# Kernel optimization log

Measured on AMD Instinct MI355X. Metric: run time of the kernel, lower is better.

## Reference

```python
import jax, jax.numpy as jnp
import numpy as np

N = 16384
N_IN = 64
N_H = 64
DIMS = [N_IN, N_H + 200, N_H + 100, N_H]  # 64 -> 264 -> 164 -> 64 (args.l == 2 path)


def setup_inputs() -> dict:
    key = jax.random.key(0)
    ks = jax.random.split(key, 16)
    inp = {
        "seq1": jax.random.normal(ks[0], (1, N, N_IN), dtype=jnp.float32),
        "seq2": jax.random.normal(ks[1], (1, N, N_IN), dtype=jnp.float32),
        # dense adjacency, scaled ~1/n like a row-normalized GCN adjacency
        "adj": jax.random.uniform(ks[2], (1, N, N), dtype=jnp.float32) / N,
        "samp_bias1": jnp.zeros((1, N), dtype=jnp.float32),
        "samp_bias2": jnp.zeros((1, N), dtype=jnp.float32),
    }
    # GCN layer params: Linear(in, out, bias=False) weight + per-layer bias
    for i in range(3):
        din, dout = DIMS[i], DIMS[i + 1]
        inp[f"w{i+1}"] = jax.random.normal(ks[3 + 2 * i], (din, dout), dtype=jnp.float32) * (1.0 / np.sqrt(din))
        inp[f"b{i+1}"] = jnp.zeros((dout,), dtype=jnp.float32)
    # Discriminator bilinear f_k = nn.Bilinear(n_h, n_h, 1): weight [n_h, n_h], bias scalar
    inp["wd"] = jax.random.normal(ks[10], (N_H, N_H), dtype=jnp.float32) * (1.0 / np.sqrt(N_H))
    inp["bd"] = jnp.zeros((), dtype=jnp.float32)
    return inp


def _encoder(seq, adj, ws, bs):
    h = seq  # [1, n, d]
    for w, b in zip(ws, bs):
        # GCN layer: act(adj @ (X W) + b)
        h = jax.nn.relu(jnp.einsum('bnm,bmd->bnd', adj, jnp.einsum('bnk,kd->bnd', h, w)) + b)
    return h


def reference(seq1, seq2, adj, samp_bias1, samp_bias2, w1, b1, w2, b2, w3, b3, wd, bd):
    ws, bs = (w1, w2, w3), (b1, b2, b3)
    h_1 = _encoder(seq1, adj, ws, bs)                 # [1, n, n_h]
    c = jax.nn.sigmoid(jnp.mean(h_1, axis=1))         # AvgReadout + sigmoid -> [1, n_h]
    h_2 = _encoder(seq2, adj, ws, bs)                 # [1, n, n_h]
    # Bilinear discriminator: sc[b, i] = h[b, i, :] @ Wd @ c[b, :] + bd (+ samp_bias)
    cw = jnp.einsum('bd,ed->be', c, wd)               # Wd acts on (h, c) pair -> [1, n_h]
    sc_1 = jnp.einsum('bnd,bd->bn', h_1, cw) + bd + samp_bias1
    sc_2 = jnp.einsum('bnd,bd->bn', h_2, cw) + bd + samp_bias2
    return jnp.concatenate([sc_1, sc_2], axis=1)      # [1, 2n]
```

## Files before the change

### kernel.cpp

```cpp
#include <hip/hip_runtime.h>
#include <hip/hip_bf16.h>

#define NN 16384

using f32x4  = __attribute__((ext_vector_type(4))) float;
using bf16x8 = __attribute__((ext_vector_type(8))) __bf16;
using u16x8  = __attribute__((ext_vector_type(8))) unsigned short;

__device__ __forceinline__ void gload_lds16(const void* g, void* l) {
  __builtin_amdgcn_global_load_lds(
      (const __attribute__((address_space(1))) unsigned*)g,
      (__attribute__((address_space(3))) unsigned*)l, 16, 0, 0);
}

__device__ __forceinline__ unsigned short bf16r(float x) {
  return __builtin_bit_cast(unsigned short, (__bf16)x);
}

__global__ void zero_cs(float* __restrict__ csS) {
  if (threadIdx.x < 128) csS[threadIdx.x] = 0.f;
}

__global__ void seqsum(const float* __restrict__ seq1, const float* __restrict__ seq2,
                       float* __restrict__ csS) {
  const int e = blockIdx.x >> 4, chunk = blockIdx.x & 15;
  const float* seq = e ? seq2 : seq1;
  const int g = threadIdx.x >> 4;
  const int q = threadIdx.x & 15;
  f32x4 acc = {};
  for (int i = 0; i < 64; ++i) {
    int r = chunk * 1024 + i * 16 + g;
    acc += *(const f32x4*)(seq + (long)r * 64 + q * 4);
  }
  __shared__ f32x4 red[256];
  red[threadIdx.x] = acc;
  __syncthreads();
  if (threadIdx.x < 64) {
    int d = threadIdx.x;
    float s = 0.f;
    #pragma unroll
    for (int g2 = 0; g2 < 16; ++g2) {
      f32x4 v = red[g2 * 16 + (d >> 2)];
      s += v[d & 3];
    }
    atomicAdd(&csS[e * 64 + d], s);
  }
}

__global__ void prep_seq(const float* __restrict__ seq1, const float* __restrict__ seq2,
                         unsigned short* __restrict__ Shi) {
  const int tid = threadIdx.x;
  const int r0  = blockIdx.x * 64;
  const float* seq = blockIdx.y ? seq2 : seq1;
  __shared__ float t[64][65];
  #pragma unroll
  for (int i = 0; i < 16; ++i) {
    int row = i * 4 + (tid >> 6);
    t[row][tid & 63] = seq[(long)(r0 + row) * 64 + (tid & 63)];
  }
  __syncthreads();
  #pragma unroll
  for (int i = 0; i < 16; ++i) {
    int col = i * 4 + (tid >> 6);
    int rr  = tid & 63;
    Shi[(long)(blockIdx.y * 64 + col) * NN + r0 + rr] = bf16r(t[rr][col]);
  }
}

__launch_bounds__(256, 3)
__global__ void gemm1(const float* __restrict__ A,
                      const unsigned short* __restrict__ Xg,
                      const float* __restrict__ cs,
                      float* __restrict__ P,
                      unsigned short* __restrict__ Vg) {
  __shared__ unsigned short As[128 * 64];
  __shared__ unsigned short Xs[2][128 * 64];
  const int tid  = threadIdx.x;
  const int lane = tid & 63;
  const int wave = tid >> 6;
  const int wr = wave & 1;
  const int wc = wave >> 1;

  int bid = blockIdx.x;
  int lin = (bid & 7) * ((int)gridDim.x >> 3) + (bid >> 3);
  const int bx = lin & 127;
  const int bz = lin >> 7;
  const int rtile = bx * 128;
  const int kbase = bz * 4096;

  const int arow0  = wave * 32 + (lane >> 3);
  const int ac     = lane & 7;
  const int awslot = ac ^ (lane >> 3);
  const float* aptr = A + (long)(rtile + arow0) * NN + kbase + ac * 8;
  unsigned short* vptr = Vg + (long)(rtile + arow0) * NN + kbase + ac * 8;

  const int cx = (lane & 7) ^ (lane >> 3);
  const unsigned short* xptr = Xg + (long)arow0 * NN + kbase + cx * 8;

  f32x4 acc[4][4] = {};
  f32x4 areg[4][2];

  #pragma unroll
  for (int t = 0; t < 4; ++t) {
    const float* ap = aptr + (long)t * 8 * NN;
    areg[t][0] = *(const f32x4*)ap;
    areg[t][1] = *(const f32x4*)(ap + 4);
    gload_lds16(xptr + (long)t * 8 * NN, &Xs[0][(wave * 4 + t) * 512]);
  }
  aptr += 64; xptr += 64;
  __syncthreads();

  int cur = 0;
  const int nsteps = 4096 / 64;
  for (int ks = 0; ks < nsteps; ++ks) {
    u16x8 wv[4];
    #pragma unroll
    for (int t = 0; t < 4; ++t) {
      #pragma unroll
      for (int i = 0; i < 8; ++i) {
        float a = (i < 4) ? areg[t][0][i] : areg[t][1][i - 4];
        wv[t][i] = bf16r(fmaf(a, 16384.f, -0.5f));
      }
      *(u16x8*)(vptr + (long)t * 8 * NN) = wv[t];
    }
    vptr += 64;
    __syncthreads();
    #pragma unroll
    for (int t = 0; t < 4; ++t)
      *(u16x8*)&As[(arow0 + t * 8) * 64 + awslot * 8] = wv[t];
    if (ks + 1 < nsteps) {
      #pragma unroll
      for (int t = 0; t < 4; ++t) {
        gload_lds16(xptr + (long)t * 8 * NN, &Xs[cur ^ 1][(wave * 4 + t) * 512]);
        const float* ap = aptr + (long)t * 8 * NN;
        areg[t][0] = *(const f32x4*)ap;
        areg[t][1] = *(const f32x4*)(ap + 4);
      }
      aptr += 64; xptr += 64;
    }
    __syncthreads();
    #pragma unroll
    for (int mk = 0; mk < 2; ++mk) {
      bf16x8 af[4];
      #pragma unroll
      for (int ni = 0; ni < 4; ++ni) {
        int ar = wr * 64 + ni * 16 + (lane & 15);
        int slot = (mk * 4 + (lane >> 4)) ^ (ar & 7);
        af[ni] = *(const bf16x8*)&As[ar * 64 + slot * 8];
      }
      #pragma unroll
      for (int mi = 0; mi < 4; ++mi) {
        int xr = wc * 64 + mi * 16 + (lane & 15);
        int slot = (mk * 4 + (lane >> 4)) ^ (xr & 7);
        bf16x8 xf = *(const bf16x8*)&Xs[cur][xr * 64 + slot * 8];
        #pragma unroll
        for (int ni = 0; ni < 4; ++ni)
          acc[mi][ni] = __builtin_amdgcn_mfma_f32_16x16x32_bf16(xf, af[ni], acc[mi][ni], 0, 0, 0);
      }
    }
    cur ^= 1;
  }

  const float scl = 1.f / 16384.f;
  float* out = P + (long)bz * 128 * NN;
  #pragma unroll
  for (int mi = 0; mi < 4; ++mi) {
    int xc = wc * 64 + mi * 16 + ((lane >> 4) << 2);
    float dc[4];
    #pragma unroll
    for (int j = 0; j < 4; ++j) dc[j] = (bz == 0) ? 0.5f * cs[xc + j] : 0.f;
    #pragma unroll
    for (int ni = 0; ni < 4; ++ni) {
      int ar = rtile + wr * 64 + ni * 16 + (lane & 15);
      #pragma unroll
      for (int j = 0; j < 4; ++j)
        out[(long)(xc + j) * NN + ar] = (acc[mi][ni][j] + dc[j]) * scl;
    }
  }
}

__launch_bounds__(256, 3)
__global__ void gemm23(const unsigned short* __restrict__ Va,
                       const unsigned short* __restrict__ Xg,
                       const float* __restrict__ cs,
                       float* __restrict__ P, int ccols, int klen, int nY) {
  __shared__ unsigned short As[128 * 64];
  __shared__ unsigned short Xs[2][128 * 64];
  const int tid  = threadIdx.x;
  const int lane = tid & 63;
  const int wave = tid >> 6;
  const int wr = wave & 1;
  const int wc = wave >> 1;

  int bid = blockIdx.x;
  int lin = (bid & 7) * ((int)gridDim.x >> 3) + (bid >> 3);
  const int by = lin % nY;
  const int bx = (lin / nY) & 127;
  const int bz = lin / (nY * 128);
  const int rtile = bx * 128;
  const int ctile = by * 128;
  const int kbase = bz * klen;

  const int arow0  = wave * 32 + (lane >> 3);
  const int ac     = lane & 7;
  const int awslot = ac ^ (lane >> 3);
  const unsigned short* aptr = Va + (long)(rtile + arow0) * NN + kbase + ac * 8;

  const int cx = (lane & 7) ^ (lane >> 3);
  const unsigned short* xptr = Xg + (long)(ctile + arow0) * NN + kbase + cx * 8;

  f32x4 acc[4][4] = {};
  u16x8 av[4];

  #pragma unroll
  for (int t = 0; t < 4; ++t) {
    av[t] = *(const u16x8*)(aptr + (long)t * 8 * NN);
    gload_lds16(xptr + (long)t * 8 * NN, &Xs[0][(wave * 4 + t) * 512]);
  }
  aptr += 64; xptr += 64;
  __syncthreads();

  int cur = 0;
  const int nsteps = klen / 64;
  for (int ks = 0; ks < nsteps; ++ks) {
    __syncthreads();
    #pragma unroll
    for (int t = 0; t < 4; ++t)
      *(u16x8*)&As[(arow0 + t * 8) * 64 + awslot * 8] = av[t];
    if (ks + 1 < nsteps) {
      #pragma unroll
      for (int t = 0; t < 4; ++t) {
        gload_lds16(xptr + (long)t * 8 * NN, &Xs[cur ^ 1][(wave * 4 + t) * 512]);
        av[t] = *(const u16x8*)(aptr + (long)t * 8 * NN);
      }
      aptr += 64; xptr += 64;
    }
    __syncthreads();
    #pragma unroll
    for (int mk = 0; mk < 2; ++mk) {
      bf16x8 af[4];
      #pragma unroll
      for (int ni = 0; ni < 4; ++ni) {
        int ar = wr * 64 + ni * 16 + (lane & 15);
        int slot = (mk * 4 + (lane >> 4)) ^ (ar & 7);
        af[ni] = *(const bf16x8*)&As[ar * 64 + slot * 8];
      }
      #pragma unroll
      for (int mi = 0; mi < 4; ++mi) {
        int xr = wc * 64 + mi * 16 + (lane & 15);
        int slot = (mk * 4 + (lane >> 4)) ^ (xr & 7);
        bf16x8 xf = *(const bf16x8*)&Xs[cur][xr * 64 + slot * 8];
        #pragma unroll
        for (int ni = 0; ni < 4; ++ni)
          acc[mi][ni] = __builtin_amdgcn_mfma_f32_16x16x32_bf16(xf, af[ni], acc[mi][ni], 0, 0, 0);
      }
    }
    cur ^= 1;
  }

  const float scl = 1.f / 16384.f;
  float* out = P + (long)bz * ccols * NN;
  #pragma unroll
  for (int mi = 0; mi < 4; ++mi) {
    int xc = ctile + wc * 64 + mi * 16 + ((lane >> 4) << 2);
    float dc[4];
    #pragma unroll
    for (int j = 0; j < 4; ++j) dc[j] = (bz == 0) ? 0.5f * cs[xc + j] : 0.f;
    #pragma unroll
    for (int ni = 0; ni < 4; ++ni) {
      int ar = rtile + wr * 64 + ni * 16 + (lane & 15);
      #pragma unroll
      for (int j = 0; j < 4; ++j)
        out[(long)(xc + j) * NN + ar] = (acc[mi][ni][j] + dc[j]) * scl;
    }
  }
}

__global__ void post1a(const float* __restrict__ P, const float* __restrict__ w1,
                       const float* __restrict__ b1, float* __restrict__ H1T) {
  const int r = blockIdx.x * 256 + threadIdx.x;
  const int e = blockIdx.y;
  for (int c = blockIdx.z * 2; c < blockIdx.z * 2 + 2; ++c) {
    const int j0 = c * 66;
    float acc[66];
    #pragma unroll
    for (int jj = 0; jj < 66; ++jj) acc[jj] = b1[j0 + jj];
    for (int k = 0; k < 64; ++k) {
      float tv = 0.f;
      #pragma unroll
      for (int z = 0; z < 4; ++z)
        tv += P[(long)(z * 128 + e * 64 + k) * NN + r];
      #pragma unroll
      for (int jj = 0; jj < 66; ++jj)
        acc[jj] = fmaf(tv, w1[k * 264 + j0 + jj], acc[jj]);
    }
    #pragma unroll
    for (int jj = 0; jj < 66; ++jj)
      H1T[(long)(e * 264 + j0 + jj) * NN + r] = fmaxf(acc[jj], 0.f);
  }
}

__global__ void post1b(const float* __restrict__ H1T, const float* __restrict__ w2,
                       unsigned short* __restrict__ G) {
  const int r  = blockIdx.x * 256 + threadIdx.x;
  const int e  = blockIdx.y;
  const int q0 = blockIdx.z * 41;
  float acc[41] = {};
  for (int j = 0; j < 264; ++j) {
    float h = H1T[(long)(e * 264 + j) * NN + r];
    #pragma unroll
    for (int qq = 0; qq < 41; ++qq)
      acc[qq] = fmaf(h, w2[j * 164 + q0 + qq], acc[qq]);
  }
  #pragma unroll
  for (int qq = 0; qq < 41; ++qq)
    G[(long)(e * 192 + q0 + qq) * NN + r] = bf16r(acc[qq]);
  if (blockIdx.z == 3) {
    for (int q = 164; q < 192; ++q)
      G[(long)(e * 192 + q) * NN + r] = 0;
  }
}

__global__ void colsum_bf16(const unsigned short* __restrict__ X, float* __restrict__ cs) {
  const int c = blockIdx.x;
  const unsigned short* row = X + (long)c * NN;
  float s = 0.f;
  for (int i = threadIdx.x; i < NN; i += 256)
    s += __uint_as_float((unsigned)row[i] << 16);
  __shared__ float red[256];
  red[threadIdx.x] = s;
  __syncthreads();
  for (int off = 128; off > 0; off >>= 1) {
    if (threadIdx.x < off) red[threadIdx.x] += red[threadIdx.x + off];
    __syncthreads();
  }
  if (threadIdx.x == 0) cs[c] = red[0];
}

__global__ void post2(const float* __restrict__ P, const float* __restrict__ w3,
                      const float* __restrict__ b2, unsigned short* __restrict__ F) {
  const int r  = blockIdx.x * 256 + threadIdx.x;
  const int e  = blockIdx.y;
  const int q0 = blockIdx.z * 32;
  float f[32] = {};
  for (int j = 0; j < 164; ++j) {
    float h = P[(long)(e * 192 + j) * NN + r] + P[(long)(384 + e * 192 + j) * NN + r] + b2[j];
    h = fmaxf(h, 0.f);
    #pragma unroll
    for (int q = 0; q < 32; ++q) f[q] = fmaf(h, w3[j * 64 + q0 + q], f[q]);
  }
  #pragma unroll
  for (int q = 0; q < 32; ++q)
    F[(long)(e * 64 + q0 + q) * NN + r] = bf16r(f[q]);
}

__global__ void post3(const float* __restrict__ P, const float* __restrict__ b3,
                      float* __restrict__ H3T) {
  const int r = blockIdx.x * 256 + threadIdx.x;
  const int e = blockIdx.y;
  #pragma unroll
  for (int q = 0; q < 64; ++q) {
    float v = b3[q];
    #pragma unroll
    for (int z = 0; z < 4; ++z)
      v += P[(long)(z * 128 + e * 64 + q) * NN + r];
    H3T[(long)(e * 64 + q) * NN + r] = fmaxf(v, 0.f);
  }
}

__global__ void colsum(const float* __restrict__ H3T, float* __restrict__ sums) {
  const int c = blockIdx.x;
  const float* row = H3T + (long)c * NN;
  float s = 0.f;
  for (int i = threadIdx.x; i < NN; i += 256) s += row[i];
  __shared__ float red[256];
  red[threadIdx.x] = s;
  __syncthreads();
  for (int off = 128; off > 0; off >>= 1) {
    if (threadIdx.x < off) red[threadIdx.x] += red[threadIdx.x + off];
    __syncthreads();
  }
  if (threadIdx.x == 0) sums[c] = red[0];
}

__global__ void make_cw(const float* __restrict__ sums, const float* __restrict__ wd,
                        float* __restrict__ cw) {
  __shared__ float cv[64];
  const int t = threadIdx.x;
  cv[t] = 1.f / (1.f + expf(-sums[t] / 16384.f));
  __syncthreads();
  float a = 0.f;
  for (int d = 0; d < 64; ++d) a += cv[d] * wd[t * 64 + d];
  cw[t] = a;
}

__global__ void score(const float* __restrict__ H3T, const float* __restrict__ cw,
                      const float* __restrict__ bdp, const float* __restrict__ sb1,
                      const float* __restrict__ sb2, float* __restrict__ out) {
  const int idx = blockIdx.x * 256 + threadIdx.x;
  const int e = idx >> 14, r = idx & (NN - 1);
  float acc = bdp[0] + (e ? sb2[r] : sb1[r]);
  const float* base = H3T + (long)e * 64 * NN + r;
  #pragma unroll
  for (int j = 0; j < 64; ++j) acc = fmaf(base[(long)j * NN], cw[j], acc);
  out[idx] = acc;
}

extern "C" void kernel_launch(void* const* d_in, const int* in_sizes, int n_in,
                              void* d_out, int out_size, void* d_ws, size_t ws_size,
                              hipStream_t stream) {
  const float* seq1 = (const float*)d_in[0];
  const float* seq2 = (const float*)d_in[1];
  const float* adj  = (const float*)d_in[2];
  const float* sb1  = (const float*)d_in[3];
  const float* sb2  = (const float*)d_in[4];
  const float* w1   = (const float*)d_in[5];
  const float* b1   = (const float*)d_in[6];
  const float* w2   = (const float*)d_in[7];
  const float* b2   = (const float*)d_in[8];
  const float* w3   = (const float*)d_in[9];
  const float* b3   = (const float*)d_in[10];
  const float* wd   = (const float*)d_in[11];
  const float* bd   = (const float*)d_in[12];
  float* out = (float*)d_out;

  char* ws = (char*)d_ws;
  unsigned short* Vg  = (unsigned short*)(ws + 0);
  unsigned short* Shi = (unsigned short*)(ws + 536870912);
  float*          Pp  = (float*)(ws + 541065216);
  unsigned short* G   = (unsigned short*)(ws + 591396864);
  float*          H1T = (float*)(ws + 603979776);
  unsigned short* F   = (unsigned short*)(ws + 638582784);
  float*          H3T = (float*)(ws + 642777088);
  float*          csS = (float*)(ws + 651165696);
  float*          csG = (float*)(ws + 651166208);
  float*          csF = (float*)(ws + 651167744);
  float*          sums= (float*)(ws + 651168256);
  float*          cw  = (float*)(ws + 651168512);

  zero_cs    <<<1, 128, 0, stream>>>(csS);
  seqsum     <<<32, 256, 0, stream>>>(seq1, seq2, csS);
  prep_seq   <<<dim3(256, 2), 256, 0, stream>>>(seq1, seq2, Shi);
  gemm1      <<<512, 256, 0, stream>>>(adj, Shi, csS, Pp, Vg);
  post1a     <<<dim3(64, 2, 2), 256, 0, stream>>>(Pp, w1, b1, H1T);
  post1b     <<<dim3(64, 2, 4), 256, 0, stream>>>(H1T, w2, G);
  colsum_bf16<<<384, 256, 0, stream>>>(G, csG);
  gemm23     <<<768, 256, 0, stream>>>(Vg, G, csG, Pp, 384, 8192, 3);
  post2      <<<dim3(64, 2, 2), 256, 0, stream>>>(Pp, w3, b2, F);
  colsum_bf16<<<128, 256, 0, stream>>>(F, csF);
  gemm23     <<<512, 256, 0, stream>>>(Vg, F, csF, Pp, 128, 4096, 1);
  post3      <<<dim3(64, 2), 256, 0, stream>>>(Pp, b3, H3T);
  colsum     <<<64, 256, 0, stream>>>(H3T, sums);
  make_cw    <<<1, 64, 0, stream>>>(sums, wd, cw);
  score      <<<128, 256, 0, stream>>>(H3T, cw, bd, sb1, sb2, out);
}
```

Baseline: 1.116 ms.

## Store centered adjacency copy as FP8 and H1T as bf16

gemm1 now writes the re-used, centered and scaled adjacency copy in an 8-bit float format (custom encoder, larger pre-scale) instead of bf16. This halves the dominant HBM traffic when gemm23 re-reads it twice. gemm23 decodes it back to bf16 in registers with packed convert instructions and rescales the result. post1a is restructured to compute the P reduction once per thread and emit bf16 H1T, which shrinks post1b's reads. Precision loss from fp8 storage of the adjacency risks accuracy, and the extra decode work adds ALU cost in the GEMM loop.

```diff
diff --git a/kernel.cpp b/kernel.cpp
--- a/kernel.cpp
+++ b/kernel.cpp
@@ -4,6 +4,7 @@
 #define NN 16384
 
 using f32x4  = __attribute__((ext_vector_type(4))) float;
+using f32x2  = __attribute__((ext_vector_type(2))) float;
 using bf16x8 = __attribute__((ext_vector_type(8))) __bf16;
 using u16x8  = __attribute__((ext_vector_type(8))) unsigned short;
 
@@ -15,6 +16,35 @@
 
 __device__ __forceinline__ unsigned short bf16r(float x) {
   return __builtin_bit_cast(unsigned short, (__bf16)x);
+}
+
+__device__ __forceinline__ unsigned fp8_enc(float f) {
+  unsigned u    = __float_as_uint(f);
+  unsigned sign = (u >> 24) & 0x80u;
+  unsigned mag  = u & 0x7FFFFFFFu;
+  unsigned e32  = mag >> 23;
+  unsigned keep = (mag >> 20) & 7u;
+  unsigned rest = mag & 0xFFFFFu;
+  unsigned r    = ((e32 - 120u) << 3) | keep;
+  r += (rest > 0x80000u) || ((rest == 0x80000u) && (keep & 1u));
+  if (e32 < 121u) r = 0u;
+  return sign | r;
+}
+
+__device__ __forceinline__ u16x8 fp8x8_to_bf16x8(uint2 r) {
+  f32x2 p0, p1, p2, p3;
+  unsigned hx = r.x >> 16, hy = r.y >> 16;
+  asm("v_cvt_pk_f32_fp8 %0, %1" : "=v"(p0) : "v"(r.x));
+  asm("v_cvt_pk_f32_fp8 %0, %1" : "=v"(p1) : "v"(hx));
+  asm("v_cvt_pk_f32_fp8 %0, %1" : "=v"(p2) : "v"(r.y));
+  asm("v_cvt_pk_f32_fp8 %0, %1" : "=v"(p3) : "v"(hy));
+  unsigned q0, q1, q2, q3;
+  asm("v_cvt_pk_bf16_f32 %0, %1, %2" : "=v"(q0) : "v"(p0.x), "v"(p0.y));
+  asm("v_cvt_pk_bf16_f32 %0, %1, %2" : "=v"(q1) : "v"(p1.x), "v"(p1.y));
+  asm("v_cvt_pk_bf16_f32 %0, %1, %2" : "=v"(q2) : "v"(p2.x), "v"(p2.y));
+  asm("v_cvt_pk_bf16_f32 %0, %1, %2" : "=v"(q3) : "v"(p3.x), "v"(p3.y));
+  uint4 qq = {q0, q1, q2, q3};
+  return __builtin_bit_cast(u16x8, qq);
 }
 
 __global__ void zero_cs(float* __restrict__ csS) {
@@ -72,7 +102,7 @@
                       const unsigned short* __restrict__ Xg,
                       const float* __restrict__ cs,
                       float* __restrict__ P,
-                      unsigned short* __restrict__ Vg) {
+                      unsigned char* __restrict__ Vg) {
   __shared__ unsigned short As[128 * 64];
   __shared__ unsigned short Xs[2][128 * 64];
   const int tid  = threadIdx.x;
@@ -92,7 +122,7 @@
   const int ac     = lane & 7;
   const int awslot = ac ^ (lane >> 3);
   const float* aptr = A + (long)(rtile + arow0) * NN + kbase + ac * 8;
-  unsigned short* vptr = Vg + (long)(rtile + arow0) * NN + kbase + ac * 8;
+  unsigned char* vptr = Vg + (long)(rtile + arow0) * NN + kbase + ac * 8;
 
   const int cx = (lane & 7) ^ (lane >> 3);
   const unsigned short* xptr = Xg + (long)arow0 * NN + kbase + cx * 8;
@@ -116,12 +146,17 @@
     u16x8 wv[4];
     #pragma unroll
     for (int t = 0; t < 4; ++t) {
+      unsigned lo = 0, hi = 0;
       #pragma unroll
       for (int i = 0; i < 8; ++i) {
-        float a = (i < 4) ? areg[t][0][i] : areg[t][1][i - 4];
-        wv[t][i] = bf16r(fmaf(a, 16384.f, -0.5f));
-      }
-      *(u16x8*)(vptr + (long)t * 8 * NN) = wv[t];
+        float a  = (i < 4) ? areg[t][0][i] : areg[t][1][i - 4];
+        float vp = fmaf(a, 1048576.f, -32.f);
+        wv[t][i] = bf16r(vp * 0.015625f);
+        unsigned b = fp8_enc(vp);
+        if (i < 4) lo |= b << (8 * i); else hi |= b << (8 * (i - 4));
+      }
+      uint2 pk = {lo, hi};
+      *(uint2*)(vptr + (long)t * 8 * NN) = pk;
     }
     vptr += 64;
     __syncthreads();
@@ -180,7 +215,7 @@
 }
 
 __launch_bounds__(256, 3)
-__global__ void gemm23(const unsigned short* __restrict__ Va,
+__global__ void gemm23(const unsigned char* __restrict__ Va,
                        const unsigned short* __restrict__ Xg,
                        const float* __restrict__ cs,
                        float* __restrict__ P, int ccols, int klen, int nY) {
@@ -204,17 +239,17 @@
   const int arow0  = wave * 32 + (lane >> 3);
   const int ac     = lane & 7;
   const int awslot = ac ^ (lane >> 3);
-  const unsigned short* aptr = Va + (long)(rtile + arow0) * NN + kbase + ac * 8;
+  const unsigned char* aptr = Va + (long)(rtile + arow0) * NN + kbase + ac * 8;
 
   const int cx = (lane & 7) ^ (lane >> 3);
   const unsigned short* xptr = Xg + (long)(ctile + arow0) * NN + kbase + cx * 8;
 
   f32x4 acc[4][4] = {};
-  u16x8 av[4];
+  uint2 raw[4];
 
   #pragma unroll
   for (int t = 0; t < 4; ++t) {
-    av[t] = *(const u16x8*)(aptr + (long)t * 8 * NN);
+    raw[t] = *(const uint2*)(aptr + (long)t * 8 * NN);
     gload_lds16(xptr + (long)t * 8 * NN, &Xs[0][(wave * 4 + t) * 512]);
   }
   aptr += 64; xptr += 64;
@@ -223,6 +258,10 @@
   int cur = 0;
   const int nsteps = klen / 64;
   for (int ks = 0; ks < nsteps; ++ks) {
+    u16x8 av[4];
+    #pragma unroll
+    for (int t = 0; t < 4; ++t)
+      av[t] = fp8x8_to_bf16x8(raw[t]);
     __syncthreads();
     #pragma unroll
     for (int t = 0; t < 4; ++t)
@@ -231,7 +270,7 @@
       #pragma unroll
       for (int t = 0; t < 4; ++t) {
         gload_lds16(xptr + (long)t * 8 * NN, &Xs[cur ^ 1][(wave * 4 + t) * 512]);
-        av[t] = *(const u16x8*)(aptr + (long)t * 8 * NN);
+        raw[t] = *(const uint2*)(aptr + (long)t * 8 * NN);
       }
       aptr += 64; xptr += 64;
     }
@@ -271,43 +310,49 @@
       int ar = rtile + wr * 64 + ni * 16 + (lane & 15);
       #pragma unroll
       for (int j = 0; j < 4; ++j)
-        out[(long)(xc + j) * NN + ar] = (acc[mi][ni][j] + dc[j]) * scl;
+        out[(long)(xc + j) * NN + ar] = (acc[mi][ni][j] * 0.015625f + dc[j]) * scl;
     }
   }
 }
 
 __global__ void post1a(const float* __restrict__ P, const float* __restrict__ w1,
-                       const float* __restrict__ b1, float* __restrict__ H1T) {
+                       const float* __restrict__ b1, unsigned short* __restrict__ H1T) {
   const int r = blockIdx.x * 256 + threadIdx.x;
   const int e = blockIdx.y;
-  for (int c = blockIdx.z * 2; c < blockIdx.z * 2 + 2; ++c) {
-    const int j0 = c * 66;
-    float acc[66];
-    #pragma unroll
-    for (int jj = 0; jj < 66; ++jj) acc[jj] = b1[j0 + jj];
+  float tv[64];
+  #pragma unroll
+  for (int k = 0; k < 64; ++k) {
+    float s = 0.f;
+    #pragma unroll
+    for (int z = 0; z < 4; ++z)
+      s += P[(long)(z * 128 + e * 64 + k) * NN + r];
+    tv[k] = s;
+  }
+  for (int c = 0; c < 8; ++c) {
+    const int j0 = c * 33;
+    float acc[33];
+    #pragma unroll
+    for (int jj = 0; jj < 33; ++jj) acc[jj] = b1[j0 + jj];
     for (int k = 0; k < 64; ++k) {
-      float tv = 0.f;
-      #pragma unroll
-      for (int z = 0; z < 4; ++z)
-        tv += P[(long)(z * 128 + e * 64 + k) * NN + r];
-      #pragma unroll
-      for (int jj = 0; jj < 66; ++jj)
-        acc[jj] = fmaf(tv, w1[k * 264 + j0 + jj], acc[jj]);
-    }
-    #pragma unroll
-    for (int jj = 0; jj < 66; ++jj)
-      H1T[(long)(e * 264 + j0 + jj) * NN + r] = fmaxf(acc[jj], 0.f);
-  }
-}
-
-__global__ void post1b(const float* __restrict__ H1T, const float* __restrict__ w2,
+      float tvk = tv[k];
+      #pragma unroll
+      for (int jj = 0; jj < 33; ++jj)
+        acc[jj] = fmaf(tvk, w1[k * 264 + j0 + jj], acc[jj]);
+    }
+    #pragma unroll
+    for (int jj = 0; jj < 33; ++jj)
+      H1T[(long)(e * 264 + j0 + jj) * NN + r] = bf16r(fmaxf(acc[jj], 0.f));
+  }
+}
+
+__global__ void post1b(const unsigned short* __restrict__ H1T, const float* __restrict__ w2,
                        unsigned short* __restrict__ G) {
   const int r  = blockIdx.x * 256 + threadIdx.x;
   const int e  = blockIdx.y;
   const int q0 = blockIdx.z * 41;
   float acc[41] = {};
   for (int j = 0; j < 264; ++j) {
-    float h = H1T[(long)(e * 264 + j) * NN + r];
+    float h = __uint_as_float((unsigned)H1T[(long)(e * 264 + j) * NN + r] << 16);
     #pragma unroll
     for (int qq = 0; qq < 41; ++qq)
       acc[qq] = fmaf(h, w2[j * 164 + q0 + qq], acc[qq]);
@@ -425,24 +470,24 @@
   float* out = (float*)d_out;
 
   char* ws = (char*)d_ws;
-  unsigned short* Vg  = (unsigned short*)(ws + 0);
-  unsigned short* Shi = (unsigned short*)(ws + 536870912);
-  float*          Pp  = (float*)(ws + 541065216);
-  unsigned short* G   = (unsigned short*)(ws + 591396864);
-  float*          H1T = (float*)(ws + 603979776);
-  unsigned short* F   = (unsigned short*)(ws + 638582784);
-  float*          H3T = (float*)(ws + 642777088);
-  float*          csS = (float*)(ws + 651165696);
-  float*          csG = (float*)(ws + 651166208);
-  float*          csF = (float*)(ws + 651167744);
-  float*          sums= (float*)(ws + 651168256);
-  float*          cw  = (float*)(ws + 651168512);
+  unsigned char*  Vg  = (unsigned char*)(ws + 0);
+  unsigned short* Shi = (unsigned short*)(ws + 268435456);
+  float*          Pp  = (float*)(ws + 272629760);
+  unsigned short* G   = (unsigned short*)(ws + 322961408);
+  unsigned short* H1T = (unsigned short*)(ws + 335544320);
+  unsigned short* F   = (unsigned short*)(ws + 352845824);
+  float*          H3T = (float*)(ws + 357040128);
+  float*          csS = (float*)(ws + 365428736);
+  float*          csG = (float*)(ws + 365429248);
+  float*          csF = (float*)(ws + 365430784);
+  float*          sums= (float*)(ws + 365431296);
+  float*          cw  = (float*)(ws + 365431552);
 
   zero_cs    <<<1, 128, 0, stream>>>(csS);
   seqsum     <<<32, 256, 0, stream>>>(seq1, seq2, csS);
   prep_seq   <<<dim3(256, 2), 256, 0, stream>>>(seq1, seq2, Shi);
   gemm1      <<<512, 256, 0, stream>>>(adj, Shi, csS, Pp, Vg);
-  post1a     <<<dim3(64, 2, 2), 256, 0, stream>>>(Pp, w1, b1, H1T);
+  post1a     <<<dim3(64, 2), 256, 0, stream>>>(Pp, w1, b1, H1T);
   post1b     <<<dim3(64, 2, 4), 256, 0, stream>>>(H1T, w2, G);
   colsum_bf16<<<384, 256, 0, stream>>>(G, csG);
   gemm23     <<<768, 256, 0, stream>>>(Vg, G, csG, Pp, 384, 8192, 3);
```

Result: slower. 1.157 ms (+3.7%).

## Double split-K in gemm1/gemm23 and store partials and H1 as bf16

Applied to the files above, without the earlier changes.

gemm1 now splits K into eight 2048-wide chunks (1024 blocks) and the first gemm23 into four 4096-wide chunks (1536 blocks), raising parallelism across CUs. Partial outputs of gemm1 and the first gemm23, plus the H1T intermediate, are written as bf16 rather than fp32, cutting write and read traffic in the post kernels, which now sum more split partials. The Vg store in gemm1 moves after the LDS write and barrier, and barriers are reordered. This adds bf16 rounding of partial sums and hidden activations, which may reduce accuracy, and adds more split-K reduction work.

```diff
diff --git a/kernel.cpp b/kernel.cpp
--- a/kernel.cpp
+++ b/kernel.cpp
@@ -15,6 +15,10 @@
 
 __device__ __forceinline__ unsigned short bf16r(float x) {
   return __builtin_bit_cast(unsigned short, (__bf16)x);
+}
+
+__device__ __forceinline__ float bf16d(unsigned short u) {
+  return __uint_as_float((unsigned)u << 16);
 }
 
 __global__ void zero_cs(float* __restrict__ csS) {
@@ -71,7 +75,7 @@
 __global__ void gemm1(const float* __restrict__ A,
                       const unsigned short* __restrict__ Xg,
                       const float* __restrict__ cs,
-                      float* __restrict__ P,
+                      unsigned short* __restrict__ P,
                       unsigned short* __restrict__ Vg) {
   __shared__ unsigned short As[128 * 64];
   __shared__ unsigned short Xs[2][128 * 64];
@@ -86,11 +90,11 @@
   const int bx = lin & 127;
   const int bz = lin >> 7;
   const int rtile = bx * 128;
-  const int kbase = bz * 4096;
+  const int kbase = bz * 2048;
 
   const int arow0  = wave * 32 + (lane >> 3);
   const int ac     = lane & 7;
-  const int awslot = ac ^ (lane >> 3);
+  const int awslot = ac ^ ((lane >> 3) & 7);
   const float* aptr = A + (long)(rtile + arow0) * NN + kbase + ac * 8;
   unsigned short* vptr = Vg + (long)(rtile + arow0) * NN + kbase + ac * 8;
 
@@ -111,7 +115,7 @@
   __syncthreads();
 
   int cur = 0;
-  const int nsteps = 4096 / 64;
+  const int nsteps = 2048 / 64;
   for (int ks = 0; ks < nsteps; ++ks) {
     u16x8 wv[4];
     #pragma unroll
@@ -121,13 +125,16 @@
         float a = (i < 4) ? areg[t][0][i] : areg[t][1][i - 4];
         wv[t][i] = bf16r(fmaf(a, 16384.f, -0.5f));
       }
-      *(u16x8*)(vptr + (long)t * 8 * NN) = wv[t];
-    }
-    vptr += 64;
+    }
     __syncthreads();
     #pragma unroll
     for (int t = 0; t < 4; ++t)
       *(u16x8*)&As[(arow0 + t * 8) * 64 + awslot * 8] = wv[t];
+    __syncthreads();
+    #pragma unroll
+    for (int t = 0; t < 4; ++t)
+      *(u16x8*)(vptr + (long)t * 8 * NN) = wv[t];
+    vptr += 64;
     if (ks + 1 < nsteps) {
       #pragma unroll
       for (int t = 0; t < 4; ++t) {
@@ -138,7 +145,6 @@
       }
       aptr += 64; xptr += 64;
     }
-    __syncthreads();
     #pragma unroll
     for (int mk = 0; mk < 2; ++mk) {
       bf16x8 af[4];
@@ -162,7 +168,7 @@
   }
 
   const float scl = 1.f / 16384.f;
-  float* out = P + (long)bz * 128 * NN;
+  unsigned short* out = P + (long)bz * 128 * NN;
   #pragma unroll
   for (int mi = 0; mi < 4; ++mi) {
     int xc = wc * 64 + mi * 16 + ((lane >> 4) << 2);
@@ -174,16 +180,17 @@
       int ar = rtile + wr * 64 + ni * 16 + (lane & 15);
       #pragma unroll
       for (int j = 0; j < 4; ++j)
-        out[(long)(xc + j) * NN + ar] = (acc[mi][ni][j] + dc[j]) * scl;
-    }
-  }
-}
-
+        out[(long)(xc + j) * NN + ar] = bf16r((acc[mi][ni][j] + dc[j]) * scl);
+    }
+  }
+}
+
+template<int OBF16>
 __launch_bounds__(256, 3)
 __global__ void gemm23(const unsigned short* __restrict__ Va,
                        const unsigned short* __restrict__ Xg,
                        const float* __restrict__ cs,
-                       float* __restrict__ P, int ccols, int klen, int nY) {
+                       void* __restrict__ Pout, int ccols, int klen, int nY) {
   __shared__ unsigned short As[128 * 64];
   __shared__ unsigned short Xs[2][128 * 64];
   const int tid  = threadIdx.x;
@@ -203,7 +210,7 @@
 
   const int arow0  = wave * 32 + (lane >> 3);
   const int ac     = lane & 7;
-  const int awslot = ac ^ (lane >> 3);
+  const int awslot = ac ^ ((lane >> 3) & 7);
   const unsigned short* aptr = Va + (long)(rtile + arow0) * NN + kbase + ac * 8;
 
   const int cx = (lane & 7) ^ (lane >> 3);
@@ -227,6 +234,7 @@
     #pragma unroll
     for (int t = 0; t < 4; ++t)
       *(u16x8*)&As[(arow0 + t * 8) * 64 + awslot * 8] = av[t];
+    __syncthreads();
     if (ks + 1 < nsteps) {
       #pragma unroll
       for (int t = 0; t < 4; ++t) {
@@ -235,7 +243,6 @@
       }
       aptr += 64; xptr += 64;
     }
-    __syncthreads();
     #pragma unroll
     for (int mk = 0; mk < 2; ++mk) {
       bf16x8 af[4];
@@ -259,7 +266,6 @@
   }
 
   const float scl = 1.f / 16384.f;
-  float* out = P + (long)bz * ccols * NN;
   #pragma unroll
   for (int mi = 0; mi < 4; ++mi) {
     int xc = ctile + wc * 64 + mi * 16 + ((lane >> 4) << 2);
@@ -270,44 +276,55 @@
     for (int ni = 0; ni < 4; ++ni) {
       int ar = rtile + wr * 64 + ni * 16 + (lane & 15);
       #pragma unroll
-      for (int j = 0; j < 4; ++j)
-        out[(long)(xc + j) * NN + ar] = (acc[mi][ni][j] + dc[j]) * scl;
-    }
-  }
-}
-
-__global__ void post1a(const float* __restrict__ P, const float* __restrict__ w1,
-                       const float* __restrict__ b1, float* __restrict__ H1T) {
+      for (int j = 0; j < 4; ++j) {
+        float v = (acc[mi][ni][j] + dc[j]) * scl;
+        if (OBF16)
+          ((unsigned short*)Pout)[(long)bz * ccols * NN + (long)(xc + j) * NN + ar] = bf16r(v);
+        else
+          ((float*)Pout)[(long)bz * ccols * NN + (long)(xc + j) * NN + ar] = v;
+      }
+    }
+  }
+}
+
+__global__ void post1a(const unsigned short* __restrict__ P, const float* __restrict__ w1,
+                       const float* __restrict__ b1, unsigned short* __restrict__ H1T) {
   const int r = blockIdx.x * 256 + threadIdx.x;
   const int e = blockIdx.y;
-  for (int c = blockIdx.z * 2; c < blockIdx.z * 2 + 2; ++c) {
-    const int j0 = c * 66;
-    float acc[66];
-    #pragma unroll
-    for (int jj = 0; jj < 66; ++jj) acc[jj] = b1[j0 + jj];
+  float tv[64];
+  #pragma unroll
+  for (int k = 0; k < 64; ++k) {
+    float s = 0.f;
+    #pragma unroll
+    for (int z = 0; z < 8; ++z)
+      s += bf16d(P[(long)(z * 128 + e * 64 + k) * NN + r]);
+    tv[k] = s;
+  }
+  for (int c = 0; c < 8; ++c) {
+    const int j0 = c * 33;
+    float acc[33];
+    #pragma unroll
+    for (int jj = 0; jj < 33; ++jj) acc[jj] = b1[j0 + jj];
     for (int k = 0; k < 64; ++k) {
-      float tv = 0.f;
-      #pragma unroll
-      for (int z = 0; z < 4; ++z)
-        tv += P[(long)(z * 128 + e * 64 + k) * NN + r];
-      #pragma unroll
-      for (int jj = 0; jj < 66; ++jj)
-        acc[jj] = fmaf(tv, w1[k * 264 + j0 + jj], acc[jj]);
-    }
-    #pragma unroll
-    for (int jj = 0; jj < 66; ++jj)
-      H1T[(long)(e * 264 + j0 + jj) * NN + r] = fmaxf(acc[jj], 0.f);
-  }
-}
-
-__global__ void post1b(const float* __restrict__ H1T, const float* __restrict__ w2,
+      float tvk = tv[k];
+      #pragma unroll
+      for (int jj = 0; jj < 33; ++jj)
+        acc[jj] = fmaf(tvk, w1[k * 264 + j0 + jj], acc[jj]);
+    }
+    #pragma unroll
+    for (int jj = 0; jj < 33; ++jj)
+      H1T[(long)(e * 264 + j0 + jj) * NN + r] = bf16r(fmaxf(acc[jj], 0.f));
+  }
+}
+
+__global__ void post1b(const unsigned short* __restrict__ H1T, const float* __restrict__ w2,
                        unsigned short* __restrict__ G) {
   const int r  = blockIdx.x * 256 + threadIdx.x;
   const int e  = blockIdx.y;
   const int q0 = blockIdx.z * 41;
   float acc[41] = {};
   for (int j = 0; j < 264; ++j) {
-    float h = H1T[(long)(e * 264 + j) * NN + r];
+    float h = bf16d(H1T[(long)(e * 264 + j) * NN + r]);
     #pragma unroll
     for (int qq = 0; qq < 41; ++qq)
       acc[qq] = fmaf(h, w2[j * 164 + q0 + qq], acc[qq]);
@@ -326,7 +343,7 @@
   const unsigned short* row = X + (long)c * NN;
   float s = 0.f;
   for (int i = threadIdx.x; i < NN; i += 256)
-    s += __uint_as_float((unsigned)row[i] << 16);
+    s += bf16d(row[i]);
   __shared__ float red[256];
   red[threadIdx.x] = s;
   __syncthreads();
@@ -337,14 +354,17 @@
   if (threadIdx.x == 0) cs[c] = red[0];
 }
 
-__global__ void post2(const float* __restrict__ P, const float* __restrict__ w3,
+__global__ void post2(const unsigned short* __restrict__ P, const float* __restrict__ w3,
                       const float* __restrict__ b2, unsigned short* __restrict__ F) {
   const int r  = blockIdx.x * 256 + threadIdx.x;
   const int e  = blockIdx.y;
   const int q0 = blockIdx.z * 32;
   float f[32] = {};
   for (int j = 0; j < 164; ++j) {
-    float h = P[(long)(e * 192 + j) * NN + r] + P[(long)(384 + e * 192 + j) * NN + r] + b2[j];
+    float h = b2[j];
+    #pragma unroll
+    for (int z = 0; z < 4; ++z)
+      h += bf16d(P[(long)(z * 384 + e * 192 + j) * NN + r]);
     h = fmaxf(h, 0.f);
     #pragma unroll
     for (int q = 0; q < 32; ++q) f[q] = fmaf(h, w3[j * 64 + q0 + q], f[q]);
@@ -427,29 +447,29 @@
   char* ws = (char*)d_ws;
   unsigned short* Vg  = (unsigned short*)(ws + 0);
   unsigned short* Shi = (unsigned short*)(ws + 536870912);
-  float*          Pp  = (float*)(ws + 541065216);
+  char*           Pp  = ws + 541065216;
   unsigned short* G   = (unsigned short*)(ws + 591396864);
-  float*          H1T = (float*)(ws + 603979776);
-  unsigned short* F   = (unsigned short*)(ws + 638582784);
-  float*          H3T = (float*)(ws + 642777088);
-  float*          csS = (float*)(ws + 651165696);
-  float*          csG = (float*)(ws + 651166208);
-  float*          csF = (float*)(ws + 651167744);
-  float*          sums= (float*)(ws + 651168256);
-  float*          cw  = (float*)(ws + 651168512);
+  unsigned short* H1T = (unsigned short*)(ws + 603979776);
+  unsigned short* F   = (unsigned short*)(ws + 621281280);
+  float*          H3T = (float*)(ws + 625475584);
+  float*          csS = (float*)(ws + 633864192);
+  float*          csG = (float*)(ws + 633864704);
+  float*          csF = (float*)(ws + 633866240);
+  float*          sums= (float*)(ws + 633866752);
+  float*          cw  = (float*)(ws + 633867008);
 
   zero_cs    <<<1, 128, 0, stream>>>(csS);
   seqsum     <<<32, 256, 0, stream>>>(seq1, seq2, csS);
   prep_seq   <<<dim3(256, 2), 256, 0, stream>>>(seq1, seq2, Shi);
-  gemm1      <<<512, 256, 0, stream>>>(adj, Shi, csS, Pp, Vg);
-  post1a     <<<dim3(64, 2, 2), 256, 0, stream>>>(Pp, w1, b1, H1T);
+  gemm1      <<<1024, 256, 0, stream>>>(adj, Shi, csS, (unsigned short*)Pp, Vg);
+  post1a     <<<dim3(64, 2), 256, 0, stream>>>((const unsigned short*)Pp, w1, b1, H1T);
   post1b     <<<dim3(64, 2, 4), 256, 0, stream>>>(H1T, w2, G);
   colsum_bf16<<<384, 256, 0, stream>>>(G, csG);
-  gemm23     <<<768, 256, 0, stream>>>(Vg, G, csG, Pp, 384, 8192, 3);
-  post2      <<<dim3(64, 2, 2), 256, 0, stream>>>(Pp, w3, b2, F);
+  gemm23<1>  <<<1536, 256, 0, stream>>>(Vg, G, csG, Pp, 384, 4096, 3);
+  post2      <<<dim3(64, 2, 2), 256, 0, stream>>>((const unsigned short*)Pp, w3, b2, F);
   colsum_bf16<<<128, 256, 0, stream>>>(F, csF);
-  gemm23     <<<512, 256, 0, stream>>>(Vg, F, csF, Pp, 128, 4096, 1);
-  post3      <<<dim3(64, 2), 256, 0, stream>>>(Pp, b3, H3T);
+  gemm23<0>  <<<512, 256, 0, stream>>>(Vg, F, csF, Pp, 128, 4096, 1);
+  post3      <<<dim3(64, 2), 256, 0, stream>>>((const float*)Pp, b3, H3T);
   colsum     <<<64, 256, 0, stream>>>(H3T, sums);
   make_cw    <<<1, 64, 0, stream>>>(sums, wd, cw);
   score      <<<128, 256, 0, stream>>>(H3T, cw, bd, sb1, sb2, out);
```

Result: slower. 1.287 ms (+15.4%).

## Load both gemm23 operands via direct global-to-LDS with 32-wide k tiles

Applied to the files above, without the earlier changes.

gemm23 now stages both the A and X operands with global_load_lds into double-buffered 32-column LDS tiles. This replaces the earlier path where A went through registers and was written to a swizzled LDS layout. The goal is to cut register traffic and one barrier per step, at the cost of twice as many k iterations and unswizzled LDS reads that may hit bank conflicts. post1a also drops its z-split, so each thread loops over all four column chunks, which halves that kernel's grid.

```diff
diff --git a/kernel.cpp b/kernel.cpp
--- a/kernel.cpp
+++ b/kernel.cpp
@@ -15,6 +15,10 @@
 
 __device__ __forceinline__ unsigned short bf16r(float x) {
   return __builtin_bit_cast(unsigned short, (__bf16)x);
+}
+
+__device__ __forceinline__ float bf16d(unsigned short u) {
+  return __uint_as_float((unsigned)u << 16);
 }
 
 __global__ void zero_cs(float* __restrict__ csS) {
@@ -90,7 +94,7 @@
 
   const int arow0  = wave * 32 + (lane >> 3);
   const int ac     = lane & 7;
-  const int awslot = ac ^ (lane >> 3);
+  const int awslot = ac ^ ((lane >> 3) & 7);
   const float* aptr = A + (long)(rtile + arow0) * NN + kbase + ac * 8;
   unsigned short* vptr = Vg + (long)(rtile + arow0) * NN + kbase + ac * 8;
 
@@ -184,8 +188,8 @@
                        const unsigned short* __restrict__ Xg,
                        const float* __restrict__ cs,
                        float* __restrict__ P, int ccols, int klen, int nY) {
-  __shared__ unsigned short As[128 * 64];
-  __shared__ unsigned short Xs[2][128 * 64];
+  __shared__ unsigned short As[2][128 * 32];
+  __shared__ unsigned short Xs[2][128 * 32];
   const int tid  = threadIdx.x;
   const int lane = tid & 63;
   const int wave = tid >> 6;
@@ -201,60 +205,48 @@
   const int ctile = by * 128;
   const int kbase = bz * klen;
 
-  const int arow0  = wave * 32 + (lane >> 3);
-  const int ac     = lane & 7;
-  const int awslot = ac ^ (lane >> 3);
-  const unsigned short* aptr = Va + (long)(rtile + arow0) * NN + kbase + ac * 8;
-
-  const int cx = (lane & 7) ^ (lane >> 3);
-  const unsigned short* xptr = Xg + (long)(ctile + arow0) * NN + kbase + cx * 8;
+  const int srow = tid >> 2;
+  const int sg   = tid & 3;
+  const unsigned short* ap = Va + (long)(rtile + srow) * NN + kbase + sg * 8;
+  const unsigned short* xp = Xg + (long)(ctile + srow) * NN + kbase + sg * 8;
 
   f32x4 acc[4][4] = {};
-  u16x8 av[4];
-
-  #pragma unroll
-  for (int t = 0; t < 4; ++t) {
-    av[t] = *(const u16x8*)(aptr + (long)t * 8 * NN);
-    gload_lds16(xptr + (long)t * 8 * NN, &Xs[0][(wave * 4 + t) * 512]);
-  }
-  aptr += 64; xptr += 64;
-  __syncthreads();
+
+  #pragma unroll
+  for (int i = 0; i < 2; ++i) {
+    gload_lds16(ap + (long)i * 64 * NN, &As[0][i * 2048 + tid * 8]);
+    gload_lds16(xp + (long)i * 64 * NN, &Xs[0][i * 2048 + tid * 8]);
+  }
+  ap += 32; xp += 32;
 
   int cur = 0;
-  const int nsteps = klen / 64;
+  const int nsteps = klen / 32;
   for (int ks = 0; ks < nsteps; ++ks) {
     __syncthreads();
-    #pragma unroll
-    for (int t = 0; t < 4; ++t)
-      *(u16x8*)&As[(arow0 + t * 8) * 64 + awslot * 8] = av[t];
     if (ks + 1 < nsteps) {
       #pragma unroll
-      for (int t = 0; t < 4; ++t) {
-        gload_lds16(xptr + (long)t * 8 * NN, &Xs[cur ^ 1][(wave * 4 + t) * 512]);
-        av[t] = *(const u16x8*)(aptr + (long)t * 8 * NN);
+      for (int i = 0; i < 2; ++i) {
+        gload_lds16(ap + (long)i * 64 * NN, &As[cur ^ 1][i * 2048 + tid * 8]);
+        gload_lds16(xp + (long)i * 64 * NN, &Xs[cur ^ 1][i * 2048 + tid * 8]);
       }
-      aptr += 64; xptr += 64;
-    }
-    __syncthreads();
-    #pragma unroll
-    for (int mk = 0; mk < 2; ++mk) {
-      bf16x8 af[4];
-      #pragma unroll
-      for (int ni = 0; ni < 4; ++ni) {
-        int ar = wr * 64 + ni * 16 + (lane & 15);
-        int slot = (mk * 4 + (lane >> 4)) ^ (ar & 7);
-        af[ni] = *(const bf16x8*)&As[ar * 64 + slot * 8];
-      }
-      #pragma unroll
-      for (int mi = 0; mi < 4; ++mi) {
-        int xr = wc * 64 + mi * 16 + (lane & 15);
-        int slot = (mk * 4 + (lane >> 4)) ^ (xr & 7);
-        bf16x8 xf = *(const bf16x8*)&Xs[cur][xr * 64 + slot * 8];
-        #pragma unroll
-        for (int ni = 0; ni < 4; ++ni)
-          acc[mi][ni] = __builtin_amdgcn_mfma_f32_16x16x32_bf16(xf, af[ni], acc[mi][ni], 0, 0, 0);
-      }
-    }
+      ap += 32; xp += 32;
+    }
+    bf16x8 af[4], xf[4];
+    #pragma unroll
+    for (int ni = 0; ni < 4; ++ni) {
+      int ar = wr * 64 + ni * 16 + (lane & 15);
+      af[ni] = *(const bf16x8*)&As[cur][ar * 32 + (lane >> 4) * 8];
+    }
+    #pragma unroll
+    for (int mi = 0; mi < 4; ++mi) {
+      int xr = wc * 64 + mi * 16 + (lane & 15);
+      xf[mi] = *(const bf16x8*)&Xs[cur][xr * 32 + (lane >> 4) * 8];
+    }
+    #pragma unroll
+    for (int mi = 0; mi < 4; ++mi)
+      #pragma unroll
+      for (int ni = 0; ni < 4; ++ni)
+        acc[mi][ni] = __builtin_amdgcn_mfma_f32_16x16x32_bf16(xf[mi], af[ni], acc[mi][ni], 0, 0, 0);
     cur ^= 1;
   }
 
@@ -280,7 +272,7 @@
                        const float* __restrict__ b1, float* __restrict__ H1T) {
   const int r = blockIdx.x * 256 + threadIdx.x;
   const int e = blockIdx.y;
-  for (int c = blockIdx.z * 2; c < blockIdx.z * 2 + 2; ++c) {
+  for (int c = 0; c < 4; ++c) {
     const int j0 = c * 66;
     float acc[66];
     #pragma unroll
@@ -326,7 +318,7 @@
   const unsigned short* row = X + (long)c * NN;
   float s = 0.f;
   for (int i = threadIdx.x; i < NN; i += 256)
-    s += __uint_as_float((unsigned)row[i] << 16);
+    s += bf16d(row[i]);
   __shared__ float red[256];
   red[threadIdx.x] = s;
   __syncthreads();
@@ -442,7 +434,7 @@
   seqsum     <<<32, 256, 0, stream>>>(seq1, seq2, csS);
   prep_seq   <<<dim3(256, 2), 256, 0, stream>>>(seq1, seq2, Shi);
   gemm1      <<<512, 256, 0, stream>>>(adj, Shi, csS, Pp, Vg);
-  post1a     <<<dim3(64, 2, 2), 256, 0, stream>>>(Pp, w1, b1, H1T);
+  post1a     <<<dim3(64, 2), 256, 0, stream>>>(Pp, w1, b1, H1T);
   post1b     <<<dim3(64, 2, 4), 256, 0, stream>>>(H1T, w2, G);
   colsum_bf16<<<384, 256, 0, stream>>>(G, csG);
   gemm23     <<<768, 256, 0, stream>>>(Vg, G, csG, Pp, 384, 8192, 3);
```

Result: slower. 1.267 ms (+13.5%).
